# Kernel optimization log

Hardware: AMD Instinct MI355X
Metric: run time of the kernel (lower is better)

## Reference

```python
import jax, jax.numpy as jnp
import numpy as np

B, W, L = 32768, 5, 20            # batch, words per example, max chars per word
WV, CV = 50000, 100               # word vocab, char vocab
CE, OC, K = 32, 30, 3             # char embed dim, conv out channels (=window_size), kernel
WE, HID, TAGS = 50, 100, 36       # word embed dim, fc1 hidden, output tags


def setup_inputs() -> dict:
    key = jax.random.key(0)
    ks = jax.random.split(key, 8)
    inp = jax.random.randint(ks[0], (B, W, 1 + L), 0, 100, dtype=jnp.int32)
    embedding_matrix = jax.random.normal(ks[1], (WV, WE), jnp.float32).at[0].set(0.0)  # padding_idx=0, frozen
    char_emb = jax.random.normal(ks[2], (CV, CE), jnp.float32).at[0].set(0.0)          # padding_idx=0
    conv_w = jax.random.normal(ks[3], (OC, CE, K), jnp.float32) * 0.1
    conv_b = jnp.zeros((OC,), jnp.float32)
    fc1_w = jax.random.normal(ks[4], (HID, (WE + OC) * W), jnp.float32) * 0.05
    fc1_b = jnp.zeros((HID,), jnp.float32)
    out_w = jax.random.normal(ks[5], (TAGS, HID), jnp.float32) * 0.1
    out_b = jnp.zeros((TAGS,), jnp.float32)
    return dict(input=inp, embedding_matrix=embedding_matrix, char_emb=char_emb,
                conv_w=conv_w, conv_b=conv_b, fc1_w=fc1_w, fc1_b=fc1_b,
                out_w=out_w, out_b=out_b)


def reference(input, embedding_matrix, char_emb, conv_w, conv_b, fc1_w, fc1_b, out_w, out_b):
    b = input.shape[0]
    word_ids = input[:, :, 0]                 # [B, W]
    char_ids = input[:, :, 1:]                # [B, W, L]
    we = embedding_matrix[word_ids]           # [B, W, 50]
    ce = char_emb[char_ids]                   # [B, W, L, CE]
    # conv1d over char axis, batched over all B*W words at once
    x = ce.reshape(b * W, L, CE).transpose(0, 2, 1)        # [B*W, CE, L]
    conv = jax.lax.conv_general_dilated(
        x, conv_w, window_strides=(1,), padding='VALID',
        dimension_numbers=('NCH', 'OIH', 'NCH')) + conv_b[None, :, None]  # [B*W, OC, L-2]
    pooled = conv.max(axis=2).reshape(b, W, OC)            # max pool over time
    feats = jnp.concatenate([we, pooled], axis=-1).reshape(b, -1)  # [B, (50+OC)*W]
    h = jnp.tanh(feats @ fc1_w.T + fc1_b)     # dropout is a no-op at inference
    return h @ out_w.T + out_b                # [B, 36]
```

## Files before the change

### kernel.cpp

```cpp
#include <hip/hip_runtime.h>

#define B_TOT 32768
#define OC 30
#define HID 100
#define TAGS 36

#define WS_TH  0
#define WS_FC1 6000
#define WS_OUT 29296

typedef __attribute__((ext_vector_type(8))) _Float16 half8;
typedef __attribute__((ext_vector_type(2))) _Float16 h2v;
typedef __attribute__((ext_vector_type(4))) float f32x4;

__device__ inline half8 ash8(uint4 u) {
    union { uint4 a; half8 b; } v; v.a = u; return v.b;
}
__device__ inline unsigned int h2u(h2v h) {
    union { h2v a; unsigned int b; } v; v.a = h; return v.b;
}
__device__ inline h2v u2h(unsigned int u) {
    union { unsigned int a; h2v b; } v; v.a = u; return v.b;
}
__device__ inline unsigned int pk_f16(float a, float b) {
    h2v h; h.x = (_Float16)a; h.y = (_Float16)b; return h2u(h);
}
__device__ inline float fast_tanh(float x) {
    float ax = __builtin_fabsf(x);
    float e  = __expf(2.0f * ax);
    float r  = 1.0f - 2.0f * __builtin_amdgcn_rcpf(e + 1.0f);
    return __builtin_copysignf(r, x);
}

__global__ void prep(const float* __restrict__ conv_w,
                     const float* __restrict__ char_emb,
                     const float* __restrict__ fc1_w,
                     const float* __restrict__ out_w,
                     unsigned int* __restrict__ ws) {
    int idx = blockIdx.x * 256 + threadIdx.x;
    if (idx < 6000) {
        int d  = idx & 3;
        int t  = idx >> 2;
        int c  = t % 100;
        int kg = t / 100;
        int g  = kg % 5, k = kg / 5;
        int rd = g * 4 + d;
        float v[2];
        #pragma unroll
        for (int e = 0; e < 2; ++e) {
            int oc = rd * 2 + e;
            float s = 0.f;
            if (oc < OC) {
                for (int ce = 0; ce < 32; ++ce)
                    s += char_emb[c * 32 + ce] * conv_w[(oc * 32 + ce) * 3 + k];
            }
            v[e] = s;
        }
        ws[WS_TH + idx] = pk_f16(v[0], v[1]);
    } else if (idx < 6000 + 23296) {
        int t = idx - 6000;
        int dw = t & 3, lane = (t >> 2) & 63, chunk = t >> 8;
        int ks = chunk % 13, nt = chunk / 13;
        int j = nt * 16 + (lane & 15);
        int k = ks * 32 + (lane >> 4) * 8 + dw * 2;
        float a = (j < HID && k     < 400) ? fc1_w[j * 400 + k]     : 0.f;
        float b = (j < HID && k + 1 < 400) ? fc1_w[j * 400 + k + 1] : 0.f;
        ws[WS_FC1 + t] = pk_f16(a, b);
    } else if (idx < 29296 + 3072) {
        int t = idx - 29296;
        int dw = t & 3, lane = (t >> 2) & 63, chunk = t >> 8;
        int ks = chunk % 4, nt = chunk / 4;
        int j = nt * 16 + (lane & 15);
        int k = ks * 32 + (lane >> 4) * 8 + dw * 2;
        float a = (j < TAGS && k     < HID) ? out_w[j * 100 + k]     : 0.f;
        float b = (j < TAGS && k + 1 < HID) ? out_w[j * 100 + k + 1] : 0.f;
        ws[WS_OUT + t] = pk_f16(a, b);
    }
}

__global__ __launch_bounds__(256, 2)
void fused(const int*   __restrict__ input,
           const float* __restrict__ emb,
           const float* __restrict__ conv_b,
           const float* __restrict__ fc1_b,
           const float* __restrict__ out_b,
           const unsigned int* __restrict__ ws,
           float*       __restrict__ out)
{
    __shared__ __align__(16) unsigned int Ths[6000];
    __shared__ __align__(16) unsigned int FL[64 * 212];

    const int tid  = threadIdx.x;
    const int wv   = tid >> 6;
    const int lane = tid & 63;
    const int ln15 = lane & 15;
    const int quad = lane >> 4;
    const int gi0  = blockIdx.x * 64 + wv * 16;
    unsigned int* Fw = &FL[wv * (16 * 212)];

    {
        const uint4* src = (const uint4*)(ws + WS_TH);
        uint4* dst = (uint4*)Ths;
        for (int idx = tid; idx < 1500; idx += 256) dst[idx] = src[idx];
    }
    __syncthreads();

    #pragma unroll
    for (int r = 0; r < 2; ++r) {
        int idx = lane + r * 64;
        Fw[(idx >> 3) * 212 + 200 + (idx & 7)] = 0;
    }

    #pragma unroll 4
    for (int idx = lane; idx < 2000; idx += 64) {
        int ph = idx % 25;
        int w  = (idx / 25) % 5;
        int i  = idx / 125;
        int wid = input[(gi0 + i) * 105 + w * 21];
        float2 e = *(const float2*)&emb[wid * 50 + ph * 2];
        Fw[i * 212 + w * 40 + ph] = pk_f16(e.x, e.y);
    }

    {
        const int q4  = lane & 3;
        const int oc0 = q4 * 8;
        h2v bias[4];
        #pragma unroll
        for (int d = 0; d < 4; ++d) {
            int a = oc0 + 2 * d, b = a + 1;
            bias[d].x = (_Float16)(a < OC ? conv_b[a] : 0.f);
            bias[d].y = (_Float16)(b < OC ? conv_b[b] : 0.f);
        }
        const unsigned int* T0 = &Ths[q4 * 400];
        const unsigned int* T1 = &Ths[q4 * 400 + 2000];
        const unsigned int* T2 = &Ths[q4 * 400 + 4000];
        #pragma unroll
        for (int it = 0; it < 5; ++it) {
            int task = (lane >> 2) + it * 16;
            int i = task / 5, w = task % 5;
            const int* cp = &input[(gi0 + i) * 105 + w * 21 + 1];
            int c[20];
            #pragma unroll
            for (int p = 0; p < 20; ++p) c[p] = cp[p];
            h2v m[4];
            #pragma unroll
            for (int d = 0; d < 4; ++d) { m[d].x = (_Float16)(-30000.f); m[d].y = (_Float16)(-30000.f); }
            #pragma unroll 6
            for (int p = 0; p < 18; ++p) {
                uint4 ra = *(const uint4*)&T0[c[p    ] * 4];
                uint4 rb = *(const uint4*)&T1[c[p + 1] * 4];
                uint4 rc = *(const uint4*)&T2[c[p + 2] * 4];
                unsigned int* pa = (unsigned int*)&ra;
                unsigned int* pb = (unsigned int*)&rb;
                unsigned int* pc = (unsigned int*)&rc;
                #pragma unroll
                for (int d = 0; d < 4; ++d) {
                    h2v s = u2h(pa[d]) + u2h(pb[d]) + u2h(pc[d]);
                    m[d] = __builtin_elementwise_max(m[d], s);
                }
            }
            int base = i * 212 + w * 40 + 25 + q4 * 4;
            Fw[base]     = h2u(m[0] + bias[0]);
            Fw[base + 1] = h2u(m[1] + bias[1]);
            Fw[base + 2] = h2u(m[2] + bias[2]);
            if (q4 < 3) Fw[base + 3] = h2u(m[3] + bias[3]);
        }
    }

    f32x4 acc[7];
    #pragma unroll
    for (int t = 0; t < 7; ++t) acc[t] = f32x4{0, 0, 0, 0};
    {
        const uint4* wp = (const uint4*)(ws + WS_FC1);
        const unsigned int* arow = &Fw[ln15 * 212 + quad * 4];
        uint4 af[13];
        #pragma unroll
        for (int ks = 0; ks < 13; ++ks) af[ks] = *(const uint4*)(arow + ks * 16);
        #pragma unroll
        for (int ks = 0; ks < 13; ++ks) {
            half8 a = ash8(af[ks]);
            #pragma unroll
            for (int t = 0; t < 7; ++t) {
                uint4 bv = wp[(t * 13 + ks) * 64 + lane];
                acc[t] = __builtin_amdgcn_mfma_f32_16x16x32_f16(a, ash8(bv), acc[t], 0, 0, 0);
            }
        }
    }

    unsigned int* Hw = Fw;
    {
        for (int t2 = lane; t2 < 224; t2 += 64) {
            int i = t2 / 14, d = t2 % 14;
            Hw[i * 68 + 50 + d] = 0;
        }
        unsigned short* Hs = (unsigned short*)Hw;
        #pragma unroll
        for (int t = 0; t < 7; ++t) {
            int j = t * 16 + ln15;
            if (j < HID) {
                float bj = fc1_b[j];
                #pragma unroll
                for (int r = 0; r < 4; ++r) {
                    int it = quad * 4 + r;
                    float hv = fast_tanh(acc[t][r] + bj);
                    _Float16 h = (_Float16)hv;
                    Hs[it * 136 + j] = *reinterpret_cast<unsigned short*>(&h);
                }
            }
        }
    }

    {
        f32x4 oacc[3];
        #pragma unroll
        for (int t = 0; t < 3; ++t) oacc[t] = f32x4{0, 0, 0, 0};
        const uint4* wpo = (const uint4*)(ws + WS_OUT);
        const int aoff = ln15 * 68 + quad * 4;
        #pragma unroll
        for (int ks = 0; ks < 4; ++ks) {
            half8 a = ash8(*(const uint4*)&Hw[aoff + ks * 16]);
            #pragma unroll
            for (int t = 0; t < 3; ++t) {
                uint4 bv = wpo[(t * 4 + ks) * 64 + lane];
                oacc[t] = __builtin_amdgcn_mfma_f32_16x16x32_f16(a, ash8(bv), oacc[t], 0, 0, 0);
            }
        }
        #pragma unroll
        for (int t = 0; t < 3; ++t) {
            int o = t * 16 + ln15;
            if (o < TAGS) {
                float bo = out_b[o];
                #pragma unroll
                for (int r = 0; r < 4; ++r) {
                    int it = gi0 + quad * 4 + r;
                    out[it * TAGS + o] = oacc[t][r] + bo;
                }
            }
        }
    }
}

extern "C" void kernel_launch(void* const* d_in, const int* in_sizes, int n_in,
                              void* d_out, int out_size, void* d_ws, size_t ws_size,
                              hipStream_t stream) {
    const int*   input  = (const int*)  d_in[0];
    const float* emb    = (const float*)d_in[1];
    const float* char_e = (const float*)d_in[2];
    const float* conv_w = (const float*)d_in[3];
    const float* conv_b = (const float*)d_in[4];
    const float* fc1_w  = (const float*)d_in[5];
    const float* fc1_b  = (const float*)d_in[6];
    const float* out_w  = (const float*)d_in[7];
    const float* out_b  = (const float*)d_in[8];
    unsigned int* ws = (unsigned int*)d_ws;

    prep<<<127, 256, 0, stream>>>(conv_w, char_e, fc1_w, out_w, ws);
    fused<<<B_TOT / 64, 256, 0, stream>>>(input, emb, conv_b, fc1_b, out_b, ws, (float*)d_out);
}
```

Baseline: 114.1 us.

## Stage fc1 and output weights through LDS with double-buffered K-slices

The prep kernel now lays out the fc1 weights k-slice-major, 2048 words per slice, and moves the output-weight offset to fit. The fused kernel loads each K-slice cooperatively across all four waves into LDS, reusing the char-table buffer, with a double buffer and register prefetch of the next slice. The output-layer weights are also staged into LDS once per block instead of each wave reading them from global memory. The aim is to cut the fourfold redundant global/L2 weight traffic per block, at the cost of 13 extra block-wide barriers in the fc1 loop. The ws buffer must be large enough for the new end offset.

```diff
diff --git a/kernel.cpp b/kernel.cpp
--- a/kernel.cpp
+++ b/kernel.cpp
@@ -7,7 +7,7 @@
 
 #define WS_TH  0
 #define WS_FC1 6000
-#define WS_OUT 29296
+#define WS_OUT 32624
 
 typedef __attribute__((ext_vector_type(8))) _Float16 half8;
 typedef __attribute__((ext_vector_type(2))) _Float16 h2v;
@@ -60,16 +60,16 @@
     } else if (idx < 6000 + 23296) {
         int t = idx - 6000;
         int dw = t & 3, lane = (t >> 2) & 63, chunk = t >> 8;
-        int ks = chunk % 13, nt = chunk / 13;
+        int ks = chunk / 7, nt = chunk % 7;
         int j = nt * 16 + (lane & 15);
         int k = ks * 32 + (lane >> 4) * 8 + dw * 2;
         float a = (j < HID && k     < 400) ? fc1_w[j * 400 + k]     : 0.f;
         float b = (j < HID && k + 1 < 400) ? fc1_w[j * 400 + k + 1] : 0.f;
-        ws[WS_FC1 + t] = pk_f16(a, b);
+        ws[WS_FC1 + ks * 2048 + (nt * 64 + lane) * 4 + dw] = pk_f16(a, b);
     } else if (idx < 29296 + 3072) {
         int t = idx - 29296;
         int dw = t & 3, lane = (t >> 2) & 63, chunk = t >> 8;
-        int ks = chunk % 4, nt = chunk / 4;
+        int ks = chunk / 3, nt = chunk % 3;
         int j = nt * 16 + (lane & 15);
         int k = ks * 32 + (lane >> 4) * 8 + dw * 2;
         float a = (j < TAGS && k     < HID) ? out_w[j * 100 + k]     : 0.f;
@@ -98,11 +98,15 @@
     const int gi0  = blockIdx.x * 64 + wv * 16;
     unsigned int* Fw = &FL[wv * (16 * 212)];
 
+    const uint4* srcB = (const uint4*)(ws + WS_FC1);
+    const int se = wv * 128 + lane;
+
     {
         const uint4* src = (const uint4*)(ws + WS_TH);
         uint4* dst = (uint4*)Ths;
         for (int idx = tid; idx < 1500; idx += 256) dst[idx] = src[idx];
     }
+    uint4 p0 = srcB[se], p1 = srcB[se + 64];
     __syncthreads();
 
     #pragma unroll
@@ -167,25 +171,45 @@
         }
     }
 
+    uint4 af[13];
+    {
+        const unsigned int* arow = &Fw[ln15 * 212 + quad * 4];
+        #pragma unroll
+        for (int ks = 0; ks < 13; ++ks) af[ks] = *(const uint4*)(arow + ks * 16);
+    }
+
     f32x4 acc[7];
     #pragma unroll
     for (int t = 0; t < 7; ++t) acc[t] = f32x4{0, 0, 0, 0};
-    {
-        const uint4* wp = (const uint4*)(ws + WS_FC1);
-        const unsigned int* arow = &Fw[ln15 * 212 + quad * 4];
-        uint4 af[13];
-        #pragma unroll
-        for (int ks = 0; ks < 13; ++ks) af[ks] = *(const uint4*)(arow + ks * 16);
-        #pragma unroll
-        for (int ks = 0; ks < 13; ++ks) {
-            half8 a = ash8(af[ks]);
-            #pragma unroll
-            for (int t = 0; t < 7; ++t) {
-                uint4 bv = wp[(t * 13 + ks) * 64 + lane];
-                acc[t] = __builtin_amdgcn_mfma_f32_16x16x32_f16(a, ash8(bv), acc[t], 0, 0, 0);
-            }
-        }
-    }
+
+    uint4* Bb = (uint4*)Ths;
+    __syncthreads();
+    Bb[se] = p0; Bb[se + 64] = p1;
+    __syncthreads();
+
+    #pragma unroll
+    for (int ks = 0; ks < 13; ++ks) {
+        uint4 n0, n1;
+        if (ks < 12) {
+            n0 = srcB[(ks + 1) * 512 + se];
+            n1 = srcB[(ks + 1) * 512 + se + 64];
+        }
+        const uint4* bp = Bb + (ks & 1) * 512;
+        half8 a = ash8(af[ks]);
+        #pragma unroll
+        for (int t = 0; t < 7; ++t)
+            acc[t] = __builtin_amdgcn_mfma_f32_16x16x32_f16(a, ash8(bp[t * 64 + lane]), acc[t], 0, 0, 0);
+        if (ks < 12) {
+            uint4* np = Bb + ((ks + 1) & 1) * 512;
+            np[se] = n0; np[se + 64] = n1;
+        }
+        __syncthreads();
+    }
+
+    const uint4* srcO = (const uint4*)(ws + WS_OUT);
+    uint4 o0 = srcO[wv * 192 + lane];
+    uint4 o1 = srcO[wv * 192 + 64 + lane];
+    uint4 o2 = srcO[wv * 192 + 128 + lane];
 
     unsigned int* Hw = Fw;
     {
@@ -210,18 +234,22 @@
         }
     }
 
+    Bb[wv * 192 + lane]       = o0;
+    Bb[wv * 192 + 64 + lane]  = o1;
+    Bb[wv * 192 + 128 + lane] = o2;
+    __syncthreads();
+
     {
         f32x4 oacc[3];
         #pragma unroll
         for (int t = 0; t < 3; ++t) oacc[t] = f32x4{0, 0, 0, 0};
-        const uint4* wpo = (const uint4*)(ws + WS_OUT);
         const int aoff = ln15 * 68 + quad * 4;
         #pragma unroll
         for (int ks = 0; ks < 4; ++ks) {
             half8 a = ash8(*(const uint4*)&Hw[aoff + ks * 16]);
             #pragma unroll
             for (int t = 0; t < 3; ++t) {
-                uint4 bv = wpo[(t * 4 + ks) * 64 + lane];
+                uint4 bv = Bb[(ks * 3 + t) * 64 + lane];
                 oacc[t] = __builtin_amdgcn_mfma_f32_16x16x32_f16(a, ash8(bv), oacc[t], 0, 0, 0);
             }
         }
```

Result: faster. 111.1 us (-2.6%).
